# Kernel tuning notes

Measured on AMD Instinct MI355X. Metric: run time of the kernel, lower is better.

## Reference

```python
import jax, jax.numpy as jnp
import numpy as np

L, B, T, C, H, V = 12, 4, 1024, 768, 12, 50257
D = C // H
SCALE = 1.0 / float(np.sqrt(D))
EPS = 1e-5


def layernorm(x, g, b):
    m = jnp.mean(x, axis=-1, keepdims=True)
    v = jnp.var(x, axis=-1, keepdims=True)
    return (x - m) / jnp.sqrt(v + EPS) * g + b


def setup_inputs() -> dict:
    key = jax.random.key(0)
    ks = jax.random.split(key, 12)
    w = lambda k, shape: jax.random.normal(k, shape, jnp.float32) * 0.02
    return {
        "idx": jax.random.randint(ks[0], (B, T), 0, V),
        "tok_emb": w(ks[1], (V, C)),
        "pos_emb": w(ks[2], (1, T, C)),
        # per-layer stacked params (leading dim L); Linear stored [in, out]
        "wq": w(ks[3], (L, C, C)), "bq": jnp.zeros((L, C)),
        "wk": w(ks[4], (L, C, C)), "bk": jnp.zeros((L, C)),
        "wv": w(ks[5], (L, C, C)), "bv": jnp.zeros((L, C)),
        "wo": w(ks[6], (L, C, C)), "bo": jnp.zeros((L, C)),
        "ln1_g": jnp.ones((L, C)), "ln1_b": jnp.zeros((L, C)),
        "ln2_g": jnp.ones((L, C)), "ln2_b": jnp.zeros((L, C)),
        "w1": w(ks[7], (L, C, 4 * C)), "b1": jnp.zeros((L, 4 * C)),
        "w2": w(ks[8], (L, 4 * C, C)), "b2": jnp.zeros((L, C)),
        "lnf_g": jnp.ones((C,)), "lnf_b": jnp.zeros((C,)),
        "head_w": w(ks[9], (C, V)),
    }


def gpt_forward(idx, tok_emb, pos_emb, wq, bq, wk, bk, wv, bv, wo, bo,
                ln1_g, ln1_b, ln2_g, ln2_b, w1, b1, w2, b2,
                lnf_g, lnf_b, head_w):
    t = idx.shape[1]
    x = tok_emb[idx] + pos_emb[:, :t, :]                     # [B,T,C]
    mask = jnp.tril(jnp.ones((t, t), dtype=bool))            # causal

    def block(x, p):
        (pwq, pbq, pwk, pbk, pwv, pbv, pwo, pbo,
         g1, be1, g2, be2, pw1, pb1, pw2, pb2) = p
        h = layernorm(x, g1, be1)
        q = (h @ pwq + pbq).reshape(B, t, H, D)
        k = (h @ pwk + pbk).reshape(B, t, H, D)
        v = (h @ pwv + pbv).reshape(B, t, H, D)
        att = jnp.einsum('bthd,bshd->bhts', q, k) * SCALE    # [B,H,T,T]
        att = jnp.where(mask, att, -jnp.inf)
        att = jax.nn.softmax(att, axis=-1)
        y = jnp.einsum('bhts,bshd->bthd', att, v).reshape(B, t, C)
        x = x + y @ pwo + pbo
        h = layernorm(x, g2, be2)
        x = x + jax.nn.gelu(h @ pw1 + pb1, approximate=False) @ pw2 + pb2
        return x, None

    x, _ = jax.lax.scan(block, x, (wq, bq, wk, bk, wv, bv, wo, bo,
                                   ln1_g, ln1_b, ln2_g, ln2_b,
                                   w1, b1, w2, b2))
    x = layernorm(x, lnf_g, lnf_b)
    return x @ head_w                                        # logits [B,T,V]


def reference(idx, tok_emb, pos_emb, wq, bq, wk, bk, wv, bv, wo, bo,
              ln1_g, ln1_b, ln2_g, ln2_b, w1, b1, w2, b2,
              lnf_g, lnf_b, head_w):
    return gpt_forward(idx, tok_emb, pos_emb, wq, bq, wk, bk, wv, bv, wo, bo,
                       ln1_g, ln1_b, ln2_g, ln2_b, w1, b1, w2, b2,
                       lnf_g, lnf_b, head_w)
```

## Files before the change

### kernel.cpp

```cpp
#include <hip/hip_runtime.h>
#include <hip/hip_bf16.h>
#include <math.h>

#define L_ 12
#define B_ 4
#define T_ 1024
#define C_ 768
#define H_ 12
#define D_ 64
#define V_ 50257
#define M_ 4096
#define QKVN 2304
#define FF_ 3072
#define VPAD_ 50432

typedef __hip_bfloat16 bf16;
typedef __attribute__((ext_vector_type(4))) float f32x4;
typedef __attribute__((ext_vector_type(8))) short short8;
typedef __attribute__((ext_vector_type(8))) __bf16 bf16x8;

typedef __attribute__((address_space(1))) void gvoid;
typedef __attribute__((address_space(3))) void svoid;

__device__ __forceinline__ f32x4 mfma_bf16(short8 a, short8 b, f32x4 c) {
  return __builtin_amdgcn_mfma_f32_16x16x32_bf16(
      __builtin_bit_cast(bf16x8, a), __builtin_bit_cast(bf16x8, b), c, 0, 0, 0);
}

__device__ __forceinline__ void gload_lds16(const void* g, void* l) {
  __builtin_amdgcn_global_load_lds((gvoid*)(void*)g, (svoid*)l, 16, 0, 0);
}

__global__ __launch_bounds__(256) void embed_kernel(const int* __restrict__ idx,
    const float* __restrict__ tok, const float* __restrict__ pos, float* __restrict__ x)
{
  const int row = blockIdx.x;
  const int t = row & (T_ - 1);
  const int id = idx[row];
  const float* te = tok + (size_t)id * C_;
  const float* pe = pos + (size_t)t * C_;
  float* xr = x + (size_t)row * C_;
  const int tid = threadIdx.x;
  xr[tid]       = te[tid]       + pe[tid];
  xr[tid + 256] = te[tid + 256] + pe[tid + 256];
  xr[tid + 512] = te[tid + 512] + pe[tid + 512];
}

__global__ __launch_bounds__(256) void ln_kernel(const float* __restrict__ x,
    const float* __restrict__ g, const float* __restrict__ be, bf16* __restrict__ out)
{
  const int row = blockIdx.x;
  const int tid = threadIdx.x;
  const float* xr = x + (size_t)row * C_;
  float v0 = xr[tid], v1 = xr[tid + 256], v2 = xr[tid + 512];
  float s = v0 + v1 + v2;
  float ss = v0 * v0 + v1 * v1 + v2 * v2;
#pragma unroll
  for (int o = 32; o >= 1; o >>= 1) { s += __shfl_xor(s, o, 64); ss += __shfl_xor(ss, o, 64); }
  __shared__ float sm[8];
  const int w = tid >> 6;
  if ((tid & 63) == 0) { sm[w] = s; sm[4 + w] = ss; }
  __syncthreads();
  s = sm[0] + sm[1] + sm[2] + sm[3];
  ss = sm[4] + sm[5] + sm[6] + sm[7];
  const float mean = s * (1.0f / C_);
  const float var = ss * (1.0f / C_) - mean * mean;
  const float rstd = rsqrtf(var + 1e-5f);
  bf16* orow = out + (size_t)row * C_;
  orow[tid]       = __float2bfloat16((v0 - mean) * rstd * g[tid]       + be[tid]);
  orow[tid + 256] = __float2bfloat16((v1 - mean) * rstd * g[tid + 256] + be[tid + 256]);
  orow[tid + 512] = __float2bfloat16((v2 - mean) * rstd * g[tid + 512] + be[tid + 512]);
}

__global__ __launch_bounds__(256) void convt_kernel(const float* __restrict__ in,
    bf16* __restrict__ out, int K, int N, long in_ls, long out_ls, int row_off)
{
  __shared__ float tile[64][65];
  in  += (size_t)blockIdx.z * in_ls;
  out += (size_t)blockIdx.z * out_ls;
  const int k0 = blockIdx.x * 64, n0 = blockIdx.y * 64;
  const int tid = threadIdx.x;
#pragma unroll
  for (int ph = 0; ph < 16; ph++) {
    int e = ph * 256 + tid;
    int lk = e >> 6, ln = e & 63;
    int gn = n0 + ln;
    tile[lk][ln] = (gn < N) ? in[(size_t)(k0 + lk) * N + gn] : 0.0f;
  }
  __syncthreads();
#pragma unroll
  for (int ph = 0; ph < 16; ph++) {
    int e = ph * 256 + tid;
    int lon = e >> 6, lok = e & 63;
    out[(size_t)(row_off + n0 + lon) * K + k0 + lok] = __float2bfloat16(tile[lok][lon]);
  }
}

__global__ __launch_bounds__(256) void packb_kernel(const float* __restrict__ bq,
    const float* __restrict__ bk, const float* __restrict__ bv, float* __restrict__ out)
{
  const int i = blockIdx.x * 256 + threadIdx.x;
  const int ly = i / QKVN, c = i % QKVN;
  float v;
  if (c < C_)            v = bq[ly * C_ + c];
  else if (c < 2 * C_)   v = bk[ly * C_ + c - C_];
  else                   v = bv[ly * C_ + c - 2 * C_];
  out[i] = v;
}

template<bool BIAS, bool GELU, bool RESID, bool BF16OUT>
__global__ __launch_bounds__(256) void gemm_bt(
    const short* __restrict__ A, const short* __restrict__ Bt,
    const float* __restrict__ bias, const float* resid,
    void* out, int M, int N, int K)
{
  __shared__ short As[128 * 64];
  __shared__ short Bs[128 * 64];
  const int tid = threadIdx.x;
  const int w = tid >> 6, l = tid & 63;
  const int l15 = l & 15, l4 = l >> 4;
  const int wr = w >> 1, wc = w & 1;
  const int nwg = gridDim.x * gridDim.y;
  const int id = blockIdx.y * gridDim.x + blockIdx.x;
  const int chunk = nwg >> 3;
  const int swz = (id & 7) * chunk + (id >> 3);
  const long m0 = (long)(swz % gridDim.x) * 128;
  const long n0 = (long)(swz / gridDim.x) * 128;

  f32x4 acc[4][4] = {};
  const int lrow8 = l >> 3;
  const int lc = l & 7;

  for (int kt = 0; kt < K; kt += 64) {
#pragma unroll
    for (int j = 0; j < 8; j++) {
      const int c = w * 8 + j;
      const int isA = (c < 16);
      const int cc = isA ? c : (c - 16);
      const int row = cc * 8 + lrow8;
      const int colsw = ((lc ^ (row & 7)) << 3);
      const short* gp = (isA ? A + (size_t)(m0 + row) * K : Bt + (size_t)(n0 + row) * K) + kt + colsw;
      short* sp = (isA ? As : Bs) + row * 64 + (lc << 3);
      gload_lds16(gp, sp);
    }
    __syncthreads();
#pragma unroll
    for (int ks = 0; ks < 2; ks++) {
      short8 af[4], bfr[4];
#pragma unroll
      for (int i = 0; i < 4; i++) {
        int row = wr * 64 + i * 16 + l15;
        int cs = (ks * 32 + l4 * 8) ^ ((row & 7) << 3);
        af[i] = *(const short8*)&As[row * 64 + cs];
      }
#pragma unroll
      for (int jn = 0; jn < 4; jn++) {
        int row = wc * 64 + jn * 16 + l15;
        int cs = (ks * 32 + l4 * 8) ^ ((row & 7) << 3);
        bfr[jn] = *(const short8*)&Bs[row * 64 + cs];
      }
#pragma unroll
      for (int i = 0; i < 4; i++)
#pragma unroll
        for (int jn = 0; jn < 4; jn++)
          acc[i][jn] = mfma_bf16(af[i], bfr[jn], acc[i][jn]);
    }
    __syncthreads();
  }

#pragma unroll
  for (int i = 0; i < 4; i++) {
    const long rbase = m0 + wr * 64 + i * 16 + l4 * 4;
#pragma unroll
    for (int jn = 0; jn < 4; jn++) {
      const long col = n0 + wc * 64 + jn * 16 + l15;
      const float bv = BIAS ? bias[col] : 0.0f;
#pragma unroll
      for (int r = 0; r < 4; r++) {
        float v = acc[i][jn][r] + bv;
        if (GELU) v = 0.5f * v * (1.0f + erff(v * 0.70710678118654752f));
        const size_t o = (size_t)(rbase + r) * (size_t)N + col;
        if (RESID)        ((float*)out)[o] = resid[o] + v;
        else if (BF16OUT) ((bf16*)out)[o] = __float2bfloat16(v);
        else              ((float*)out)[o] = v;
      }
    }
  }
}

__global__ __launch_bounds__(512, 2) void gemm256(const short* __restrict__ A,
    const short* __restrict__ Bt, float* __restrict__ out, int Mb, int N, int K)
{
  __shared__ short As[2][256 * 64];
  __shared__ short Bs[2][256 * 64];
  const int tid = threadIdx.x;
  const int l = tid & 63;
  const int l15 = l & 15, l4 = l >> 4;
  const int wv = tid >> 6;
  const int wm = wv >> 2, wn = wv & 3;
  const int nwg = gridDim.x;
  const int chunk = nwg >> 3;
  const int bid = blockIdx.x;
  const int swz = (bid & 7) * chunk + (bid >> 3);
  const long m0 = (long)(swz % Mb) * 256;
  const long n0 = (long)(swz / Mb) * 256;
  const int nkt = K >> 6;
  const int rr = tid >> 3, g = tid & 7;

  f32x4 acc[8][4] = {};

  auto stage = [&](int s, int kt) {
    const int kb = kt << 6;
#pragma unroll
    for (int ph = 0; ph < 4; ph++) {
      const int r = ph * 64 + rr;
      const int cg = ((g ^ (r & 7)) << 3);
      gload_lds16(A  + (size_t)(m0 + r) * K + kb + cg, &As[s][r * 64 + g * 8]);
      gload_lds16(Bt + (size_t)(n0 + r) * K + kb + cg, &Bs[s][r * 64 + g * 8]);
    }
  };

  stage(0, 0);
  asm volatile("s_waitcnt vmcnt(0)" ::: "memory");
  __builtin_amdgcn_s_barrier();

  int cur = 0;
  for (int kt = 0; kt < nkt; ++kt) {
    if (kt + 1 < nkt) stage(cur ^ 1, kt + 1);
#pragma unroll
    for (int ks = 0; ks < 2; ks++) {
      short8 bfr[4];
#pragma unroll
      for (int j = 0; j < 4; j++) {
        int row = wn * 64 + j * 16 + l15;
        int cs = (ks * 32 + l4 * 8) ^ ((row & 7) << 3);
        bfr[j] = *(const short8*)&Bs[cur][row * 64 + cs];
      }
#pragma unroll
      for (int i = 0; i < 8; i++) {
        int row = wm * 128 + i * 16 + l15;
        int cs = (ks * 32 + l4 * 8) ^ ((row & 7) << 3);
        short8 af = *(const short8*)&As[cur][row * 64 + cs];
#pragma unroll
        for (int j = 0; j < 4; j++)
          acc[i][j] = mfma_bf16(af, bfr[j], acc[i][j]);
      }
    }
    asm volatile("s_waitcnt vmcnt(0)" ::: "memory");
    __builtin_amdgcn_s_barrier();
    cur ^= 1;
  }

#pragma unroll
  for (int i = 0; i < 8; i++) {
#pragma unroll
    for (int j = 0; j < 4; j++) {
      const long col = n0 + wn * 64 + j * 16 + l15;
      if (col >= N) continue;
#pragma unroll
      for (int r = 0; r < 4; r++) {
        const long row = m0 + wm * 128 + i * 16 + l4 * 4 + r;
        out[(size_t)row * (size_t)N + col] = acc[i][j][r];
      }
    }
  }
}

__global__ __launch_bounds__(256) void repack_kv(const short* __restrict__ qkv,
    short* __restrict__ kt, short* __restrict__ vt)
{
  __shared__ short tile[64][72];
  const int t0 = blockIdx.x * 64, bh = blockIdx.y;
  const int b = bh / H_, h = bh % H_;
  const int tid = threadIdx.x;
#pragma unroll
  for (int ph = 0; ph < 2; ph++) {
    int r = ph * 32 + (tid >> 3), cg = (tid & 7) * 8;
    short8 v = *(const short8*)&qkv[(size_t)(b * T_ + t0 + r) * QKVN + C_ + h * D_ + cg];
    *(short8*)&kt[((size_t)bh * T_ + t0 + r) * 64 + cg] = v;
  }
#pragma unroll
  for (int ph = 0; ph < 2; ph++) {
    int lt = ph * 32 + (tid >> 3);
    int ld = (tid & 7) * 8;
    short8 v = *(const short8*)&qkv[(size_t)(b * T_ + t0 + lt) * QKVN + 2 * C_ + h * D_ + ld];
#pragma unroll
    for (int j = 0; j < 8; j++) tile[lt][ld + j] = v[j];
  }
  __syncthreads();
#pragma unroll
  for (int ph = 0; ph < 2; ph++) {
    int ldd = ph * 32 + (tid >> 3);
    int ltt = (tid & 7) * 8;
    short8 v;
#pragma unroll
    for (int j = 0; j < 8; j++) v[j] = tile[ltt + j][ldd];
    *(short8*)&vt[((size_t)bh * D_ + ldd) * T_ + t0 + ltt] = v;
  }
}

__global__ __launch_bounds__(256) void attn_kernel(const short* __restrict__ qkv,
    const short* __restrict__ kt, const short* __restrict__ vt, bf16* __restrict__ y)
{
  __shared__ short Ks[2][64 * 64];
  __shared__ short Vs[2][64 * 64];
  __shared__ bf16 P[64 * 72];
  const int qt = blockIdx.x, bh = blockIdx.y;
  const int b = bh / H_, h = bh % H_;
  const int tid = threadIdx.x, w = tid >> 6, l = tid & 63;
  const int l15 = l & 15, l4 = l >> 4;
  const int qrow0 = qt * 64 + w * 16;
  const float SC2 = 0.125f * 1.44269504088896f;

  auto stageKV = [&](int s, int s0) {
    const short* ksrc = kt + ((size_t)bh * T_ + s0) * 64;
    const short* vsrc = vt + (size_t)bh * D_ * T_ + s0;
#pragma unroll
    for (int ph = 0; ph < 2; ph++) {
      int r = ph * 32 + (tid >> 3);
      int cg = ((tid & 7) ^ (r & 7)) << 3;
      gload_lds16(ksrc + (size_t)r * 64 + cg, &Ks[s][r * 64 + (tid & 7) * 8]);
      gload_lds16(vsrc + (size_t)r * T_ + cg, &Vs[s][r * 64 + (tid & 7) * 8]);
    }
  };

  short8 qf[2];
#pragma unroll
  for (int kf = 0; kf < 2; kf++)
    qf[kf] = *(const short8*)&qkv[(size_t)(b * T_ + qrow0 + l15) * QKVN + h * D_ + kf * 32 + l4 * 8];

  f32x4 O[4] = {};
  float mst[4], lst[4];
#pragma unroll
  for (int r = 0; r < 4; r++) { mst[r] = -1e30f; lst[r] = 0.0f; }

  stageKV(0, 0);
  __syncthreads();

  int cur = 0;
  const int send = qt * 64 + 64;
  for (int s0 = 0; s0 < send; s0 += 64) {
    if (s0 + 64 < send) stageKV(cur ^ 1, s0 + 64);
    f32x4 S[4];
#pragma unroll
    for (int cf = 0; cf < 4; cf++) {
      const int row = cf * 16 + l15;
      const int c0 = (l4 * 8) ^ ((row & 7) << 3);
      const int c1 = (32 + l4 * 8) ^ ((row & 7) << 3);
      short8 k0 = *(const short8*)&Ks[cur][row * 64 + c0];
      short8 k1 = *(const short8*)&Ks[cur][row * 64 + c1];
      f32x4 z = {0.0f, 0.0f, 0.0f, 0.0f};
      z = mfma_bf16(qf[0], k0, z);
      z = mfma_bf16(qf[1], k1, z);
      S[cf] = z;
    }
#pragma unroll
    for (int cf = 0; cf < 4; cf++)
#pragma unroll
      for (int r = 0; r < 4; r++) {
        const int i = qrow0 + l4 * 4 + r;
        const int jc = s0 + cf * 16 + l15;
        const float v = S[cf][r] * SC2;
        S[cf][r] = (jc <= i) ? v : -1e30f;
      }
    float mx[4], al[4], rs[4];
#pragma unroll
    for (int r = 0; r < 4; r++) {
      float m_ = fmaxf(fmaxf(S[0][r], S[1][r]), fmaxf(S[2][r], S[3][r]));
#pragma unroll
      for (int o = 1; o < 16; o <<= 1) m_ = fmaxf(m_, __shfl_xor(m_, o, 64));
      const float mn = fmaxf(mst[r], m_);
      al[r] = exp2f(mst[r] - mn);
      mst[r] = mn;
      mx[r] = mn;
      rs[r] = 0.0f;
    }
#pragma unroll
    for (int cf = 0; cf < 4; cf++)
#pragma unroll
      for (int r = 0; r < 4; r++) {
        const float pv = exp2f(S[cf][r] - mx[r]);
        rs[r] += pv;
        P[(w * 16 + l4 * 4 + r) * 72 + cf * 16 + l15] = __float2bfloat16(pv);
      }
#pragma unroll
    for (int r = 0; r < 4; r++) {
      float t = rs[r];
#pragma unroll
      for (int o = 1; o < 16; o <<= 1) t += __shfl_xor(t, o, 64);
      lst[r] = lst[r] * al[r] + t;
#pragma unroll
      for (int df = 0; df < 4; df++) O[df][r] *= al[r];
    }
    short8 pa[2];
#pragma unroll
    for (int sf = 0; sf < 2; sf++)
      pa[sf] = *(const short8*)&P[(w * 16 + l15) * 72 + sf * 32 + l4 * 8];
#pragma unroll
    for (int df = 0; df < 4; df++) {
      const int row = df * 16 + l15;
      const int c0 = (l4 * 8) ^ ((row & 7) << 3);
      const int c1 = (32 + l4 * 8) ^ ((row & 7) << 3);
      short8 v0 = *(const short8*)&Vs[cur][row * 64 + c0];
      short8 v1 = *(const short8*)&Vs[cur][row * 64 + c1];
      O[df] = mfma_bf16(pa[0], v0, O[df]);
      O[df] = mfma_bf16(pa[1], v1, O[df]);
    }
    __syncthreads();
    cur ^= 1;
  }

#pragma unroll
  for (int r = 0; r < 4; r++) {
    const float inv = 1.0f / lst[r];
    const size_t row = (size_t)(b * T_ + qrow0 + l4 * 4 + r);
#pragma unroll
    for (int df = 0; df < 4; df++)
      y[row * C_ + h * D_ + df * 16 + l15] = __float2bfloat16(O[df][r] * inv);
  }
}

extern "C" void kernel_launch(void* const* d_in, const int* in_sizes, int n_in,
                              void* d_out, int out_size, void* d_ws, size_t ws_size,
                              hipStream_t stream)
{
  const int*   idx  = (const int*)d_in[0];
  const float* tok  = (const float*)d_in[1];
  const float* pos  = (const float*)d_in[2];
  const float* wq   = (const float*)d_in[3];
  const float* bq   = (const float*)d_in[4];
  const float* wk   = (const float*)d_in[5];
  const float* bk   = (const float*)d_in[6];
  const float* wv   = (const float*)d_in[7];
  const float* bv   = (const float*)d_in[8];
  const float* wo   = (const float*)d_in[9];
  const float* bo   = (const float*)d_in[10];
  const float* ln1g = (const float*)d_in[11];
  const float* ln1b = (const float*)d_in[12];
  const float* ln2g = (const float*)d_in[13];
  const float* ln2b = (const float*)d_in[14];
  const float* w1   = (const float*)d_in[15];
  const float* b1   = (const float*)d_in[16];
  const float* w2   = (const float*)d_in[17];
  const float* b2   = (const float*)d_in[18];
  const float* lnfg = (const float*)d_in[19];
  const float* lnfb = (const float*)d_in[20];
  const float* headw= (const float*)d_in[21];

  char* p = (char*)d_ws;
  size_t off = 0;
  auto alloc = [&](size_t n) { void* r = p + off; off += (n + 255) & ~(size_t)255; return r; };
  short* qkvT  = (short*)alloc((size_t)L_ * QKVN * C_ * 2);
  short* woT   = (short*)alloc((size_t)L_ * C_ * C_ * 2);
  short* w1T   = (short*)alloc((size_t)L_ * FF_ * C_ * 2);
  short* w2T   = (short*)alloc((size_t)L_ * C_ * FF_ * 2);
  short* headT = (short*)alloc((size_t)VPAD_ * C_ * 2);
  float* qkvb  = (float*)alloc((size_t)L_ * QKVN * 4);
  float* x     = (float*)alloc((size_t)M_ * C_ * 4);
  bf16*  h     = (bf16*)alloc((size_t)M_ * C_ * 2);
  short* qkvB  = (short*)alloc((size_t)M_ * QKVN * 2);
  short* kt    = (short*)alloc((size_t)B_ * H_ * T_ * D_ * 2);
  short* vt    = (short*)alloc((size_t)B_ * H_ * D_ * T_ * 2);
  short* y     = (short*)alloc((size_t)M_ * C_ * 2);
  short* hid   = (short*)alloc((size_t)M_ * FF_ * 2);
  if (off > ws_size) return;

  convt_kernel<<<dim3(12, 12, 12), 256, 0, stream>>>(wq, (bf16*)qkvT, C_, C_, (long)C_ * C_, (long)QKVN * C_, 0);
  convt_kernel<<<dim3(12, 12, 12), 256, 0, stream>>>(wk, (bf16*)qkvT, C_, C_, (long)C_ * C_, (long)QKVN * C_, C_);
  convt_kernel<<<dim3(12, 12, 12), 256, 0, stream>>>(wv, (bf16*)qkvT, C_, C_, (long)C_ * C_, (long)QKVN * C_, 2 * C_);
  convt_kernel<<<dim3(12, 12, 12), 256, 0, stream>>>(wo, (bf16*)woT, C_, C_, (long)C_ * C_, (long)C_ * C_, 0);
  convt_kernel<<<dim3(12, 48, 12), 256, 0, stream>>>(w1, (bf16*)w1T, C_, FF_, (long)C_ * FF_, (long)FF_ * C_, 0);
  convt_kernel<<<dim3(48, 12, 12), 256, 0, stream>>>(w2, (bf16*)w2T, FF_, C_, (long)FF_ * C_, (long)C_ * FF_, 0);
  convt_kernel<<<dim3(12, VPAD_ / 64, 1), 256, 0, stream>>>(headw, (bf16*)headT, C_, V_, 0, 0, 0);
  packb_kernel<<<dim3(108), 256, 0, stream>>>(bq, bk, bv, qkvb);

  embed_kernel<<<dim3(M_), 256, 0, stream>>>(idx, tok, pos, x);

  for (int ly = 0; ly < L_; ly++) {
    ln_kernel<<<dim3(M_), 256, 0, stream>>>(x, ln1g + ly * C_, ln1b + ly * C_, h);
    gemm_bt<true, false, false, true><<<dim3(32, 18), 256, 0, stream>>>(
        (const short*)h, qkvT + (size_t)ly * QKVN * C_, qkvb + ly * QKVN, nullptr, qkvB, M_, QKVN, C_);
    repack_kv<<<dim3(16, 48), 256, 0, stream>>>(qkvB, kt, vt);
    attn_kernel<<<dim3(16, 48), 256, 0, stream>>>(qkvB, kt, vt, (bf16*)y);
    gemm_bt<true, false, true, false><<<dim3(32, 6), 256, 0, stream>>>(
        y, woT + (size_t)ly * C_ * C_, bo + ly * C_, x, x, M_, C_, C_);
    ln_kernel<<<dim3(M_), 256, 0, stream>>>(x, ln2g + ly * C_, ln2b + ly * C_, h);
    gemm_bt<true, true, false, true><<<dim3(32, 24), 256, 0, stream>>>(
        (const short*)h, w1T + (size_t)ly * FF_ * C_, b1 + ly * FF_, nullptr, hid, M_, FF_, C_);
    gemm_bt<true, false, true, false><<<dim3(32, 6), 256, 0, stream>>>(
        hid, w2T + (size_t)ly * C_ * FF_, b2 + ly * C_, x, x, M_, C_, FF_);
  }

  ln_kernel<<<dim3(M_), 256, 0, stream>>>(x, lnfg, lnfb, h);
  gemm256<<<dim3((M_ / 256) * (VPAD_ / 256)), 512, 0, stream>>>(
      (const short*)h, headT, (float*)d_out, M_ / 256, V_, C_);
}
```

Baseline: 3.728 ms.

## Restructure 256x256 GEMM into ping-pong phased pipeline and use it for QKV/FFN1

```diff
diff --git a/kernel.cpp b/kernel.cpp
--- a/kernel.cpp
+++ b/kernel.cpp
@@ -188,20 +188,18 @@
   }
 }
 
-__global__ __launch_bounds__(512, 2) void gemm256(const short* __restrict__ A,
-    const short* __restrict__ Bt, float* __restrict__ out, int Mb, int N, int K)
+template<bool BIAS, bool GELU, bool BF16OUT, bool BOUND>
+__global__ __launch_bounds__(512, 1) void gemm256(
+    const short* __restrict__ A, const short* __restrict__ Bt,
+    const float* __restrict__ bias, void* out, int Mb, int N, int K)
 {
   __shared__ short As[2][256 * 64];
   __shared__ short Bs[2][256 * 64];
   const int tid = threadIdx.x;
-  const int l = tid & 63;
-  const int l15 = l & 15, l4 = l >> 4;
-  const int wv = tid >> 6;
-  const int wm = wv >> 2, wn = wv & 3;
-  const int nwg = gridDim.x;
-  const int chunk = nwg >> 3;
-  const int bid = blockIdx.x;
-  const int swz = (bid & 7) * chunk + (bid >> 3);
+  const int l = tid & 63, l15 = l & 15, l4 = l >> 4;
+  const int wv = tid >> 6, wm = wv >> 2, wn = wv & 3;
+  const int nwg = gridDim.x, chunkx = nwg >> 3, bid = blockIdx.x;
+  const int swz = (bid & 7) * chunkx + (bid >> 3);
   const long m0 = (long)(swz % Mb) * 256;
   const long n0 = (long)(swz / Mb) * 256;
   const int nkt = K >> 6;
@@ -209,46 +207,108 @@
 
   f32x4 acc[8][4] = {};
 
-  auto stage = [&](int s, int kt) {
-    const int kb = kt << 6;
-#pragma unroll
-    for (int ph = 0; ph < 4; ph++) {
-      const int r = ph * 64 + rr;
-      const int cg = ((g ^ (r & 7)) << 3);
-      gload_lds16(A  + (size_t)(m0 + r) * K + kb + cg, &As[s][r * 64 + g * 8]);
-      gload_lds16(Bt + (size_t)(n0 + r) * K + kb + cg, &Bs[s][r * 64 + g * 8]);
+  auto stA = [&](int s, int kt, int off) {
+#pragma unroll
+    for (int p = 0; p < 2; p++) {
+      const int r = p * 128 + off + rr;
+      gload_lds16(A + (size_t)(m0 + r) * K + (kt << 6) + ((g ^ (r & 7)) << 3),
+                  &As[s][r * 64 + g * 8]);
     }
   };
-
-  stage(0, 0);
-  asm volatile("s_waitcnt vmcnt(0)" ::: "memory");
+  auto stB = [&](int s, int kt, int off) {
+#pragma unroll
+    for (int p = 0; p < 2; p++) {
+      const int r = p * 128 + ((rr >> 5) << 6) + (rr & 31) + off;
+      gload_lds16(Bt + (size_t)(n0 + r) * K + (kt << 6) + ((g ^ (r & 7)) << 3),
+                  &Bs[s][r * 64 + g * 8]);
+    }
+  };
+  auto rdA = [&](int s, int mf, int ks) {
+    const int row = wm * 128 + mf * 16 + l15;
+    const int cs = (ks * 32 + l4 * 8) ^ ((row & 7) << 3);
+    return *(const short8*)&As[s][row * 64 + cs];
+  };
+  auto rdB = [&](int s, int nf, int ks) {
+    const int row = wn * 64 + nf * 16 + l15;
+    const int cs = (ks * 32 + l4 * 8) ^ ((row & 7) << 3);
+    return *(const short8*)&Bs[s][row * 64 + cs];
+  };
+
+  stA(0, 0, 0);  stB(0, 0, 0);
+  stA(0, 0, 64); stB(0, 0, 32);
+  asm volatile("s_waitcnt vmcnt(4)" ::: "memory");
   __builtin_amdgcn_s_barrier();
 
-  int cur = 0;
-  for (int kt = 0; kt < nkt; ++kt) {
-    if (kt + 1 < nkt) stage(cur ^ 1, kt + 1);
+  int q = 0;
+  for (int kt = 0; kt < nkt; ++kt, q ^= 1) {
+    const int ktn = (kt + 1 < nkt) ? kt + 1 : kt;
+    short8 a0[2][4], a1[2][4], b0[2][2], b1[2][2];
+
 #pragma unroll
     for (int ks = 0; ks < 2; ks++) {
-      short8 bfr[4];
-#pragma unroll
-      for (int j = 0; j < 4; j++) {
-        int row = wn * 64 + j * 16 + l15;
-        int cs = (ks * 32 + l4 * 8) ^ ((row & 7) << 3);
-        bfr[j] = *(const short8*)&Bs[cur][row * 64 + cs];
-      }
-#pragma unroll
-      for (int i = 0; i < 8; i++) {
-        int row = wm * 128 + i * 16 + l15;
-        int cs = (ks * 32 + l4 * 8) ^ ((row & 7) << 3);
-        short8 af = *(const short8*)&As[cur][row * 64 + cs];
-#pragma unroll
-        for (int j = 0; j < 4; j++)
-          acc[i][j] = mfma_bf16(af, bfr[j], acc[i][j]);
-      }
-    }
-    asm volatile("s_waitcnt vmcnt(0)" ::: "memory");
-    __builtin_amdgcn_s_barrier();
-    cur ^= 1;
+#pragma unroll
+      for (int f = 0; f < 4; f++) a0[ks][f] = rdA(q, f, ks);
+#pragma unroll
+      for (int j = 0; j < 2; j++) b0[ks][j] = rdB(q, j, ks);
+    }
+    stA(q ^ 1, ktn, 0); stB(q ^ 1, ktn, 0);
+    __builtin_amdgcn_s_barrier();
+    __builtin_amdgcn_s_setprio(1);
+#pragma unroll
+    for (int f = 0; f < 4; f++)
+#pragma unroll
+      for (int j = 0; j < 2; j++) {
+        acc[f][j] = mfma_bf16(a0[0][f], b0[0][j], acc[f][j]);
+        acc[f][j] = mfma_bf16(a0[1][f], b0[1][j], acc[f][j]);
+      }
+    __builtin_amdgcn_s_setprio(0);
+    asm volatile("s_waitcnt vmcnt(4)" ::: "memory");
+    __builtin_amdgcn_s_barrier();
+
+#pragma unroll
+    for (int ks = 0; ks < 2; ks++)
+#pragma unroll
+      for (int f = 0; f < 4; f++) a1[ks][f] = rdA(q, f + 4, ks);
+    __builtin_amdgcn_s_barrier();
+    __builtin_amdgcn_s_setprio(1);
+#pragma unroll
+    for (int f = 0; f < 4; f++)
+#pragma unroll
+      for (int j = 0; j < 2; j++) {
+        acc[f + 4][j] = mfma_bf16(a1[0][f], b0[0][j], acc[f + 4][j]);
+        acc[f + 4][j] = mfma_bf16(a1[1][f], b0[1][j], acc[f + 4][j]);
+      }
+    __builtin_amdgcn_s_setprio(0);
+    __builtin_amdgcn_s_barrier();
+
+#pragma unroll
+    for (int ks = 0; ks < 2; ks++)
+#pragma unroll
+      for (int j = 0; j < 2; j++) b1[ks][j] = rdB(q, j + 2, ks);
+    stA(q ^ 1, ktn, 64); stB(q ^ 1, ktn, 32);
+    __builtin_amdgcn_s_barrier();
+    __builtin_amdgcn_s_setprio(1);
+#pragma unroll
+    for (int f = 0; f < 4; f++)
+#pragma unroll
+      for (int j = 0; j < 2; j++) {
+        acc[f][j + 2] = mfma_bf16(a0[0][f], b1[0][j], acc[f][j + 2]);
+        acc[f][j + 2] = mfma_bf16(a0[1][f], b1[1][j], acc[f][j + 2]);
+      }
+    __builtin_amdgcn_s_setprio(0);
+    __builtin_amdgcn_s_barrier();
+
+    __builtin_amdgcn_s_setprio(1);
+#pragma unroll
+    for (int f = 0; f < 4; f++)
+#pragma unroll
+      for (int j = 0; j < 2; j++) {
+        acc[f + 4][j + 2] = mfma_bf16(a1[0][f], b1[0][j], acc[f + 4][j + 2]);
+        acc[f + 4][j + 2] = mfma_bf16(a1[1][f], b1[1][j], acc[f + 4][j + 2]);
+      }
+    __builtin_amdgcn_s_setprio(0);
+    asm volatile("s_waitcnt vmcnt(4)" ::: "memory");
+    __builtin_amdgcn_s_barrier();
   }
 
 #pragma unroll
@@ -256,11 +316,15 @@
 #pragma unroll
     for (int j = 0; j < 4; j++) {
       const long col = n0 + wn * 64 + j * 16 + l15;
-      if (col >= N) continue;
+      if (BOUND && col >= N) continue;
+      const float bv = BIAS ? bias[col] : 0.0f;
 #pragma unroll
       for (int r = 0; r < 4; r++) {
         const long row = m0 + wm * 128 + i * 16 + l4 * 4 + r;
-        out[(size_t)row * (size_t)N + col] = acc[i][j][r];
+        float v = acc[i][j][r] + bv;
+        if (GELU) v = 0.5f * v * (1.0f + erff(v * 0.70710678118654752f));
+        if (BF16OUT) ((bf16*)out)[(size_t)row * (size_t)N + col] = __float2bfloat16(v);
+        else         ((float*)out)[(size_t)row * (size_t)N + col] = v;
       }
     }
   }
@@ -478,20 +542,20 @@
 
   for (int ly = 0; ly < L_; ly++) {
     ln_kernel<<<dim3(M_), 256, 0, stream>>>(x, ln1g + ly * C_, ln1b + ly * C_, h);
-    gemm_bt<true, false, false, true><<<dim3(32, 18), 256, 0, stream>>>(
-        (const short*)h, qkvT + (size_t)ly * QKVN * C_, qkvb + ly * QKVN, nullptr, qkvB, M_, QKVN, C_);
+    gemm256<true, false, true, false><<<dim3((M_ / 256) * (QKVN / 256)), 512, 0, stream>>>(
+        (const short*)h, qkvT + (size_t)ly * QKVN * C_, qkvb + ly * QKVN, qkvB, M_ / 256, QKVN, C_);
     repack_kv<<<dim3(16, 48), 256, 0, stream>>>(qkvB, kt, vt);
     attn_kernel<<<dim3(16, 48), 256, 0, stream>>>(qkvB, kt, vt, (bf16*)y);
     gemm_bt<true, false, true, false><<<dim3(32, 6), 256, 0, stream>>>(
         y, woT + (size_t)ly * C_ * C_, bo + ly * C_, x, x, M_, C_, C_);
     ln_kernel<<<dim3(M_), 256, 0, stream>>>(x, ln2g + ly * C_, ln2b + ly * C_, h);
-    gemm_bt<true, true, false, true><<<dim3(32, 24), 256, 0, stream>>>(
-        (const short*)h, w1T + (size_t)ly * FF_ * C_, b1 + ly * FF_, nullptr, hid, M_, FF_, C_);
+    gemm256<true, true, true, false><<<dim3((M_ / 256) * (FF_ / 256)), 512, 0, stream>>>(
+        (const short*)h, w1T + (size_t)ly * FF_ * C_, b1 + ly * FF_, hid, M_ / 256, FF_, C_);
     gemm_bt<true, false, true, false><<<dim3(32, 6), 256, 0, stream>>>(
         hid, w2T + (size_t)ly * C_ * FF_, b2 + ly * C_, x, x, M_, C_, FF_);
   }
 
   ln_kernel<<<dim3(M_), 256, 0, stream>>>(x, lnfg, lnfb, h);
-  gemm256<<<dim3((M_ / 256) * (VPAD_ / 256)), 512, 0, stream>>>(
-      (const short*)h, headT, (float*)d_out, M_ / 256, V_, C_);
-}
+  gemm256<false, false, false, true><<<dim3((M_ / 256) * (VPAD_ / 256)), 512, 0, stream>>>(
+      (const short*)h, headT, nullptr, d_out, M_ / 256, V_, C_);
+}
```

After: 3.880 ms. +4.1%, slower.
